# Kernel optimization log

Hardware: AMD Instinct MI355X
Metric: run time of the kernel (lower is better)

Reference implementation:

```python
import jax, jax.numpy as jnp
import numpy as np

EPS = 1.1920929e-07  # torch F.rms_norm default eps for fp32
D, NH, NKV, HD = 1024, 16, 4, 64
MLP_MULT, L = 3, 6           # L = num_layers // 2 shared blocks
VS, HS, LS, ROPE_B = 50257, 4096, 30.0, 10000.0
B, S = 2, 2048


def rmsn(x):
    return x * jax.lax.rsqrt(jnp.mean(jnp.square(x), -1, keepdims=True) + EPS)


def rope_tables(s):
    f = 1.0 / ROPE_B ** (jnp.arange(0, HD, 2, dtype=jnp.float32) / HD)
    fr = jnp.outer(jnp.arange(s, dtype=jnp.float32), f)  # [s, HD/2]
    return jnp.cos(fr), jnp.sin(fr)


def rot(x, c, s):
    h = x.shape[-1] // 2
    x1, x2 = x[..., :h], x[..., h:]
    return jnp.concatenate([x1 * c + x2 * s, -x1 * s + x2 * c], -1)


def attn(x, Wq, Wk, Wv, Wo, qg, cos, sin):
    b, s, d = x.shape
    q = (x @ Wq.T).reshape(b, s, NH, HD).swapaxes(1, 2)    # [b,nh,s,hd]
    k = (x @ Wk.T).reshape(b, s, NKV, HD).swapaxes(1, 2)   # [b,nkv,s,hd]
    v = (x @ Wv.T).reshape(b, s, NKV, HD).swapaxes(1, 2)
    q, k = rmsn(q), rmsn(k)                                # QK RMSNorm (no weight)
    c, si = cos[None, None], sin[None, None]
    q, k = rot(q, c, si), rot(k, c, si)
    q = q * qg[None, :, None, None]                        # per-head gate
    g = NH // NKV
    qr = q.reshape(b, NKV, g, s, HD)
    scores = jnp.einsum('bkgqd,bksd->bkgqs', qr, k) / jnp.sqrt(jnp.float32(HD))
    mask = jnp.tril(jnp.ones((s, s), bool))
    scores = jnp.where(mask, scores, -jnp.inf)
    p = jax.nn.softmax(scores, -1)
    y = jnp.einsum('bkgqs,bksd->bkgqd', p, v).reshape(b, NH, s, HD)
    y = y.swapaxes(1, 2).reshape(b, s, d)
    return y @ Wo.T


def mlp(x, Wf, Wo2):
    return jnp.square(jax.nn.relu(x @ Wf.T)) @ Wo2.T       # ReLU^2 MLP


def block(x, x0, p, cos, sin):
    Wq, Wk, Wv, Wo, qg, a_sc, m_sc, rm, Wf, Wo2 = p
    x = rm[0] * x + rm[1] * x0                             # learned residual mix
    x = x + a_sc * attn(rmsn(x), Wq, Wk, Wv, Wo, qg, cos, sin)
    x = x + m_sc * mlp(rmsn(x), Wf, Wo2)
    return x


def setup_inputs() -> dict:
    key = jax.random.key(0)
    ks = jax.random.split(key, 16)
    sd = 0.02
    return {
        'ids': jax.random.randint(ks[0], (B, S), 0, VS, dtype=jnp.int32),
        'y': jax.random.randint(ks[1], (B, S), 0, VS, dtype=jnp.int32),
        'u_emb': jax.random.normal(ks[2], (VS, D // 2), jnp.float32) * 0.02,
        'b_emb': jax.random.normal(ks[3], (HS, D // 2), jnp.float32) * 0.01,
        'Wq': jax.random.normal(ks[4], (L, D, D), jnp.float32) * sd,
        'Wk': jax.random.normal(ks[5], (L, NKV * HD, D), jnp.float32) * sd,
        'Wv': jax.random.normal(ks[6], (L, NKV * HD, D), jnp.float32) * sd,
        'Wo': jax.random.normal(ks[7], (L, D, D), jnp.float32) * sd,
        'qg': jnp.ones((L, NH), jnp.float32),
        'a_scale': jnp.ones((L, D), jnp.float32),
        'm_scale': jnp.ones((L, D), jnp.float32),
        'rm': jnp.stack([jnp.full((L, D), 0.7, jnp.float32), jnp.full((L, D), 0.3, jnp.float32)], 1),
        'Wf': jax.random.normal(ks[8], (L, MLP_MULT * D, D), jnp.float32) * sd,
        'Wo2': jax.random.normal(ks[9], (L, D, MLP_MULT * D), jnp.float32) * sd,
        'sw': jnp.ones((L, D), jnp.float32),
    }


def reference(ids, y, u_emb, b_emb, Wq, Wk, Wv, Wo, qg, a_scale, m_scale, rm, Wf, Wo2, sw):
    b, s = ids.shape
    # BigramHash embedding: (prev_id*VS + id) % HS, computed mod-HS to stay in int32
    pi = jnp.pad(ids[:, :-1], ((0, 0), (1, 0)))
    bi = (((pi % HS) * (VS % HS)) % HS + ids % HS) % HS
    h = jnp.concatenate([u_emb[ids], b_emb[bi]], -1)       # [b,s,D]
    h = rmsn(h)
    cos, sin = rope_tables(s)
    h0, sk = h, []
    for i in range(L):                                     # encoder half
        p = (Wq[i], Wk[i], Wv[i], Wo[i], qg[i], a_scale[i], m_scale[i], rm[i], Wf[i], Wo2[i])
        h = block(h, h0, p, cos, sin)
        sk.append(h)
    for i in range(L):                                     # decoder half (reversed blocks, skips)
        h = h + sw[i] * sk[L - 1 - i]
        j = L - 1 - i
        p = (Wq[j], Wk[j], Wv[j], Wo[j], qg[j], a_scale[j], m_scale[j], rm[j], Wf[j], Wo2[j])
        h = block(h, h0, p, cos, sin)
    h = rmsn(h)
    # tied bigram-hash head: out_weight = [u_emb | zeros]  ->  only first D/2 dims matter
    lg = h.reshape(-1, D)[:, :D // 2] @ u_emb.T            # [b*s, VS]
    lg = LS * jnp.tanh(lg / LS)                            # logit softcap
    logp = jax.nn.log_softmax(lg.astype(jnp.float32), -1)
    yf = y.reshape(-1)
    loss = -jnp.mean(jnp.take_along_axis(logp, yf[:, None], 1)[:, 0])
    return loss
```

## Files before the change

### kernel.cpp

```cpp
#include <hip/hip_runtime.h>
#include <cstdint>
#include <cstddef>

constexpr int   Dm    = 1024;
constexpr int   NHn   = 16;
constexpr int   NKVn  = 4;
constexpr int   HDn   = 64;
constexpr int   Ln    = 6;
constexpr int   Sn    = 2048;
constexpr int   Bn    = 2;
constexpr int   ROWS  = Bn * Sn;
constexpr int   VSn   = 50257;
constexpr int   HSn   = 4096;
constexpr float EPSF  = 1.1920929e-07f;
constexpr int   VCHUNK = 4096;
constexpr int   VPAD   = 50304;
constexpr float LOG2E  = 1.44269504f;

#define DEV __device__ __forceinline__

typedef __attribute__((ext_vector_type(8))) short bf16x8;
typedef __attribute__((ext_vector_type(4))) float f32x4;
using ush = unsigned short;

DEV ush f2bf(float f) {
    unsigned int u = __float_as_uint(f);
    u = (u + 0x7fffu + ((u >> 16) & 1u)) >> 16;
    return (ush)u;
}

DEV float b2f(ush v) {
    return __uint_as_float(((unsigned int)v) << 16);
}

DEV f32x4 mfma16(bf16x8 a, bf16x8 b, f32x4 c) {
    return __builtin_amdgcn_mfma_f32_16x16x32_bf16(a, b, c, 0, 0, 0);
}

DEV void llds16(const ush* g, ush* l) {
    __builtin_amdgcn_global_load_lds(
        (const __attribute__((address_space(1))) void*)g,
        (__attribute__((address_space(3))) void*)l, 16, 0, 0);
}

DEV void bar() {
    asm volatile("" ::: "memory");
    __builtin_amdgcn_s_barrier();
    asm volatile("" ::: "memory");
}

DEV float block_sum256(float v, float* red) {
#pragma unroll
    for (int off = 32; off; off >>= 1) v += __shfl_xor(v, off);
    __syncthreads();
    if ((threadIdx.x & 63) == 0) red[threadIdx.x >> 6] = v;
    __syncthreads();
    return red[0] + red[1] + red[2] + red[3];
}

DEV float block_max256(float v, float* red) {
#pragma unroll
    for (int off = 32; off; off >>= 1) v = fmaxf(v, __shfl_xor(v, off));
    __syncthreads();
    if ((threadIdx.x & 63) == 0) red[threadIdx.x >> 6] = v;
    __syncthreads();
    return fmaxf(fmaxf(red[0], red[1]), fmaxf(red[2], red[3]));
}

__global__ void rope_kernel(float* __restrict__ cb, float* __restrict__ sb) {
    int idx = blockIdx.x * 256 + threadIdx.x;
    if (idx >= Sn * 32) return;
    int t = idx >> 5, f = idx & 31;
    float freq = powf(10000.f, -(float)f * (1.f / 32.f));
    float ang  = (float)t * freq;
    cb[idx] = cosf(ang);
    sb[idx] = sinf(ang);
}

__global__ void cvt_bf16_kernel(const float* __restrict__ s, ush* __restrict__ d, int n4) {
    int i = blockIdx.x * 256 + threadIdx.x;
    if (i >= n4) return;
    float4 v = *(const float4*)(s + (size_t)i * 4);
    ushort4 o;
    o.x = f2bf(v.x); o.y = f2bf(v.y); o.z = f2bf(v.z); o.w = f2bf(v.w);
    *(ushort4*)(d + (size_t)i * 4) = o;
}

__global__ void zpad_kernel(ush* __restrict__ p, int n) {
    int i = blockIdx.x * 256 + threadIdx.x;
    if (i < n) p[i] = 0;
}

__global__ __launch_bounds__(256)
void embed_kernel(const int* __restrict__ ids, const float* __restrict__ ue,
                  const float* __restrict__ be, float* __restrict__ h,
                  float* __restrict__ h0) {
    __shared__ float red[4];
    int r = blockIdx.x;
    int s = r % Sn;
    int id = ids[r];
    int prev = (s == 0) ? 0 : ids[r - 1];
    int bi = ((prev % HSn) * (VSn % HSn) % HSn + id % HSn) % HSn;
    int tid = threadIdx.x;
    float vals[4];
    float ss = 0.f;
#pragma unroll
    for (int t = 0; t < 4; ++t) {
        int j = tid + t * 256;
        float v = (j < 512) ? ue[(size_t)id * 512 + j]
                            : be[(size_t)bi * 512 + (j - 512)];
        vals[t] = v; ss += v * v;
    }
    ss = block_sum256(ss, red);
    float rinv = rsqrtf(ss * (1.f / Dm) + EPSF);
#pragma unroll
    for (int t = 0; t < 4; ++t) {
        int j = tid + t * 256;
        float v = vals[t] * rinv;
        h [(size_t)r * Dm + j] = v;
        h0[(size_t)r * Dm + j] = v;
    }
}

template<bool SKIP>
__global__ __launch_bounds__(256)
void resmix_kernel(float* __restrict__ h, const float* __restrict__ h0,
                   const float* __restrict__ rm0, ush* __restrict__ xnb,
                   const ush* __restrict__ skb, const float* __restrict__ sw) {
    __shared__ float red[4];
    int r = blockIdx.x, tid = threadIdx.x;
    const float* rm1 = rm0 + Dm;
    float vals[4]; float ss = 0.f;
#pragma unroll
    for (int t = 0; t < 4; ++t) {
        int j = tid + t * 256;
        size_t o = (size_t)r * Dm + j;
        float base = h[o];
        if (SKIP) base = fmaf(sw[j], b2f(skb[o]), base);
        float v = rm0[j] * base + rm1[j] * h0[o];
        vals[t] = v; ss += v * v;
        h[o] = v;
    }
    ss = block_sum256(ss, red);
    float rinv = rsqrtf(ss * (1.f / Dm) + EPSF);
#pragma unroll
    for (int t = 0; t < 4; ++t)
        xnb[(size_t)r * Dm + tid + t * 256] = f2bf(vals[t] * rinv);
}

__global__ __launch_bounds__(256)
void rmsn_kernel(const float* __restrict__ x, ush* __restrict__ out) {
    __shared__ float red[4];
    int r = blockIdx.x, tid = threadIdx.x;
    float vals[4]; float ss = 0.f;
#pragma unroll
    for (int t = 0; t < 4; ++t) {
        float v = x[(size_t)r * Dm + tid + t * 256];
        vals[t] = v; ss += v * v;
    }
    ss = block_sum256(ss, red);
    float rinv = rsqrtf(ss * (1.f / Dm) + EPSF);
#pragma unroll
    for (int t = 0; t < 4; ++t)
        out[(size_t)r * Dm + tid + t * 256] = f2bf(vals[t] * rinv);
}

template<int TM, int MODE>
__global__ __launch_bounds__(256)
void gemm_k(const ush* __restrict__ A, const ush* __restrict__ B,
            ush* __restrict__ C, int M, int N, int K,
            int lda, int ldb, int ldc,
            float* __restrict__ hres, const float* __restrict__ sc,
            ush* __restrict__ dup) {
    constexpr int ASZ = TM * 32;
    __shared__ __align__(16) ush As[3][ASZ];
    __shared__ __align__(16) ush Bs[3][128 * 32];
    const int m0 = blockIdx.x * TM, n0 = blockIdx.y * 128;
    const int tid  = threadIdx.x;
    const int w    = tid >> 6, lane = tid & 63;
    const int l15  = lane & 15, quad = lane >> 4;
    const int wr   = w >> 1, wc = w & 1;
    constexpr int NI = TM / 32;

    const int srow = lane >> 2;
    const int schs = (lane & 3) ^ ((srow >> 1) & 3);
    const ush* Ag;
    int aoff;
    if constexpr (TM == 128) {
        Ag   = A + (size_t)(m0 + w * 32 + srow) * lda + schs * 8;
        aoff = w * 1024;
    } else {
        Ag   = A + (size_t)(m0 + w * 16 + srow) * lda + schs * 8;
        aoff = w * 512;
    }
    const ush* Bg  = B + (size_t)(n0 + w * 32 + srow) * ldb + schs * 8;
    const int boff = w * 1024;

    auto stage = [&](int buf, int k0) {
        llds16(Ag + k0, &As[buf][aoff]);
        if constexpr (TM == 128) llds16(Ag + k0 + 16 * lda, &As[buf][aoff + 512]);
        llds16(Bg + k0,            &Bs[buf][boff]);
        llds16(Bg + k0 + 16 * ldb, &Bs[buf][boff + 512]);
    };

    f32x4 acc[NI][4] = {};
    const int nt = K >> 5;

    stage(0, 0);
    if (nt > 1) {
        stage(1, 32);
        if constexpr (TM == 128) asm volatile("s_waitcnt vmcnt(4)" ::: "memory");
        else                     asm volatile("s_waitcnt vmcnt(3)" ::: "memory");
    } else {
        asm volatile("s_waitcnt vmcnt(0)" ::: "memory");
    }
    bar();

    const int cso = (quad ^ ((l15 >> 1) & 3)) * 8;
    int bcur = 0;
    for (int t = 0; t < nt; ++t) {
        if (t + 2 < nt) {
            int bn = bcur >= 1 ? bcur - 1 : 2;
            stage(bn, (t + 2) * 32);
        }
        bf16x8 af[NI], bfv[4];
#pragma unroll
        for (int i = 0; i < NI; ++i)
            af[i] = *(const bf16x8*)&As[bcur][(wr * (TM / 2) + i * 16 + l15) * 32 + cso];
#pragma unroll
        for (int j = 0; j < 4; ++j)
            bfv[j] = *(const bf16x8*)&Bs[bcur][(wc * 64 + j * 16 + l15) * 32 + cso];
#pragma unroll
        for (int i = 0; i < NI; ++i)
#pragma unroll
            for (int j = 0; j < 4; ++j)
                acc[i][j] = mfma16(af[i], bfv[j], acc[i][j]);
        if (t + 2 < nt) {
            if constexpr (TM == 128) asm volatile("s_waitcnt vmcnt(4)" ::: "memory");
            else                     asm volatile("s_waitcnt vmcnt(3)" ::: "memory");
        } else {
            asm volatile("s_waitcnt vmcnt(0)" ::: "memory");
        }
        bar();
        bcur = bcur == 2 ? 0 : bcur + 1;
    }

#pragma unroll
    for (int i = 0; i < NI; ++i) {
#pragma unroll
        for (int j = 0; j < 4; ++j) {
            int row = m0 + wr * (TM / 2) + i * 16 + quad * 4;
            int col = n0 + wc * 64 + j * 16 + l15;
#pragma unroll
            for (int r = 0; r < 4; ++r) {
                float v = acc[i][j][r];
                if (MODE == 1) { v = fmaxf(v, 0.f); v = v * v; }
                else if (MODE == 2) {
                    float ax = fabsf(v) * (1.f / 30.f);
                    float e  = __expf(-2.f * ax);
                    float t  = (1.f - e) / (1.f + e);
                    v = copysignf(t * 30.f, v);
                }
                if (MODE == 3) {
                    size_t o = (size_t)(row + r) * ldc + col;
                    float nv = fmaf(sc[col], v, hres[o]);
                    hres[o] = nv;
                    if (dup) dup[o] = f2bf(nv);
                } else {
                    C[(size_t)(row + r) * ldc + col] = f2bf(v);
                }
            }
        }
    }
}

__global__ __launch_bounds__(256)
void qknorm_rope_kernel(const ush* __restrict__ in,
                        ush* __restrict__ qout, ush* __restrict__ kout,
                        const float* __restrict__ cosb, const float* __restrict__ sinb,
                        const float* __restrict__ qg) {
    int idx  = blockIdx.x * 4 + (threadIdx.x >> 6);
    int lane = threadIdx.x & 63;
    int t, hh, in_off;
    ush* outp; int out_ld;
    bool isq = idx < ROWS * NHn;
    if (isq) { t = idx >> 4; hh = idx & 15; in_off = hh * 64; outp = qout; out_ld = 1024; }
    else { int i2 = idx - ROWS * NHn; t = i2 >> 2; hh = i2 & 3; in_off = 1024 + hh * 64; outp = kout; out_ld = 256; }
    int sidx = t % Sn;
    float x = b2f(in[(size_t)t * 1536 + in_off + lane]);
    float ss = x * x;
#pragma unroll
    for (int off = 32; off; off >>= 1) ss += __shfl_xor(ss, off);
    float xn = x * rsqrtf(ss * (1.f / HDn) + EPSF);
    float partner = __shfl_xor(xn, 32);
    int f = lane & 31;
    float c  = cosb[sidx * 32 + f];
    float sv = sinb[sidx * 32 + f];
    float o = (lane < 32) ? fmaf(xn, c, partner * sv)
                          : fmaf(xn, c, -partner * sv);
    if (isq) o *= qg[hh] * (0.125f * LOG2E);
    outp[(size_t)t * out_ld + hh * 64 + lane] = f2bf(o);
}

__global__ __launch_bounds__(256)
void vtrans_kernel(const ush* __restrict__ in, ush* __restrict__ out) {
    __shared__ ush tile[32][33];
    int s0 = blockIdx.x * 32;
    int c0 = blockIdx.y * 32;
    int i = threadIdx.x >> 5;
    int j = threadIdx.x & 31;
#pragma unroll
    for (int k = 0; k < 4; ++k)
        tile[i + k * 8][j] = in[(size_t)(s0 + i + k * 8) * 1536 + 1280 + c0 + j];
    __syncthreads();
#pragma unroll
    for (int k = 0; k < 4; ++k)
        out[(size_t)(c0 + i + k * 8) * (size_t)ROWS + s0 + j] = tile[j][i + k * 8];
}

__global__ __launch_bounds__(256)
void attn_mfma_kernel(const ush* __restrict__ qb,
                      const ush* __restrict__ kb,
                      const ush* __restrict__ vt,
                      ush* __restrict__ opart,
                      float* __restrict__ lpart,
                      const float* __restrict__ qgl) {
    __shared__ __align__(16) ush Ks[64 * 72];
    __shared__ __align__(16) ush Vs[64 * 72];
    __shared__ __align__(16) unsigned int PsD[128 * 36];
    const int pair = blockIdx.x % 40;
    const int bh   = blockIdx.x / 40;
    const int h    = bh & 15;
    const int b    = bh >> 4;
    const int g    = (pair >= 24) ? 3 : (pair >= 12) ? 2 : (pair >= 4) ? 1 : 0;
    const int off_p = pair - 2 * g * (g + 1);
    const int t    = 4 * g + off_p / (g + 1);
    const int c    = off_p % (g + 1);
    const int kvh  = h >> 2;
    const int w    = threadIdx.x >> 6, lane = threadIdx.x & 63;
    const int l15  = lane & 15, quad = lane >> 4;
    const int q0   = t * 128;
    const int k_lo = c * 512;
    const int k_hi_full = (t + 1) * 128;
    const int k_hi = (k_lo + 512 < k_hi_full) ? (k_lo + 512) : k_hi_full;
    const int nblk = (k_hi - k_lo) >> 6;
    const float mfix = 8.f * fabsf(qgl[h]) * LOG2E;

    bf16x8 qf[2][2];
    {
        size_t qr = (size_t)(b * Sn + q0 + w * 32 + l15) * 1024 + h * 64;
        qf[0][0] = *(const bf16x8*)(qb + qr + quad * 8);
        qf[0][1] = *(const bf16x8*)(qb + qr + 32 + quad * 8);
        qf[1][0] = *(const bf16x8*)(qb + qr + 16 * 1024 + quad * 8);
        qf[1][1] = *(const bf16x8*)(qb + qr + 16 * 1024 + 32 + quad * 8);
    }
    f32x4 Oacc[2][4] = {};
    float lsum[2][4] = {{0.f,0.f,0.f,0.f},{0.f,0.f,0.f,0.f}};

    const int rrS = threadIdx.x >> 3, chS = threadIdx.x & 7;
    const size_t kbase = (size_t)(b * Sn) * 256 + kvh * 64;
    const size_t vbase = (size_t)(kvh * 64) * (size_t)ROWS + b * Sn;

    uint4 kr0 = *(const uint4*)(kb + kbase + (size_t)(k_lo + rrS) * 256 + chS * 8);
    uint4 kr1 = *(const uint4*)(kb + kbase + (size_t)(k_lo + rrS + 32) * 256 + chS * 8);
    uint4 vr0 = *(const uint4*)(vt + vbase + (size_t)rrS * ROWS + k_lo + chS * 8);
    uint4 vr1 = *(const uint4*)(vt + vbase + (size_t)(rrS + 32) * ROWS + k_lo + chS * 8);

    for (int kb_i = 0; kb_i < nblk; ++kb_i) {
        const int k0 = k_lo + kb_i * 64;
        __syncthreads();
        *(uint4*)&Ks[rrS * 72 + chS * 8]        = kr0;
        *(uint4*)&Ks[(rrS + 32) * 72 + chS * 8] = kr1;
        *(uint4*)&Vs[rrS * 72 + chS * 8]        = vr0;
        *(uint4*)&Vs[(rrS + 32) * 72 + chS * 8] = vr1;
        __syncthreads();
        if (kb_i + 1 < nblk) {
            int k0n = k0 + 64;
            kr0 = *(const uint4*)(kb + kbase + (size_t)(k0n + rrS) * 256 + chS * 8);
            kr1 = *(const uint4*)(kb + kbase + (size_t)(k0n + rrS + 32) * 256 + chS * 8);
            vr0 = *(const uint4*)(vt + vbase + (size_t)rrS * ROWS + k0n + chS * 8);
            vr1 = *(const uint4*)(vt + vbase + (size_t)(rrS + 32) * ROWS + k0n + chS * 8);
        }

        f32x4 S0[4] = {}, S1[4] = {};
#pragma unroll
        for (int cc = 0; cc < 4; ++cc) {
            bf16x8 kf0 = *(const bf16x8*)&Ks[(cc * 16 + l15) * 72 + quad * 8];
            bf16x8 kf1 = *(const bf16x8*)&Ks[(cc * 16 + l15) * 72 + 32 + quad * 8];
            S0[cc] = mfma16(qf[0][0], kf0, S0[cc]);
            S0[cc] = mfma16(qf[0][1], kf1, S0[cc]);
            S1[cc] = mfma16(qf[1][0], kf0, S1[cc]);
            S1[cc] = mfma16(qf[1][1], kf1, S1[cc]);
        }

#pragma unroll
        for (int f = 0; f < 2; ++f) {
            f32x4* S = f ? S1 : S0;
            const int qbF = q0 + w * 32 + f * 16;
            if (k0 + 63 > qbF) {
#pragma unroll
                for (int cc = 0; cc < 4; ++cc) {
                    int key = k0 + cc * 16 + l15;
#pragma unroll
                    for (int r = 0; r < 4; ++r)
                        if (key > qbF + quad * 4 + r) S[cc][r] = -INFINITY;
                }
            }
#pragma unroll
            for (int cc = 0; cc < 4; ++cc)
#pragma unroll
                for (int r = 0; r < 4; ++r) {
                    float p = exp2f(S[cc][r] - mfix);
                    S[cc][r] = p;
                    lsum[f][r] += p;
                }
            const int prow = w * 32 + f * 16 + quad * 4;
#pragma unroll
            for (int cp = 0; cp < 2; ++cp)
#pragma unroll
                for (int r = 0; r < 4; ++r) {
                    unsigned int pk = __builtin_amdgcn_perm(
                        __float_as_uint(S[cp + 2][r]), __float_as_uint(S[cp][r]),
                        0x07060302u);
                    PsD[(prow + r) * 36 + cp * 16 + l15] = pk;
                }
        }

#pragma unroll
        for (int f = 0; f < 2; ++f) {
            const int prow = w * 32 + f * 16 + l15;
            unsigned int d[8];
            *(uint4*)&d[0] = *(const uint4*)&PsD[prow * 36 + quad * 8];
            *(uint4*)&d[4] = *(const uint4*)&PsD[prow * 36 + quad * 8 + 4];
            unsigned int lo[4], hi[4];
#pragma unroll
            for (int tt = 0; tt < 4; ++tt) {
                lo[tt] = __builtin_amdgcn_perm(d[2 * tt + 1], d[2 * tt], 0x05040100u);
                hi[tt] = __builtin_amdgcn_perm(d[2 * tt + 1], d[2 * tt], 0x07060302u);
            }
            bf16x8 pf0 = *(const bf16x8*)lo;
            bf16x8 pf1 = *(const bf16x8*)hi;
#pragma unroll
            for (int dt = 0; dt < 4; ++dt) {
                bf16x8 vf0 = *(const bf16x8*)&Vs[(dt * 16 + l15) * 72 + quad * 8];
                bf16x8 vf1 = *(const bf16x8*)&Vs[(dt * 16 + l15) * 72 + 32 + quad * 8];
                Oacc[f][dt] = mfma16(pf0, vf0, Oacc[f][dt]);
                Oacc[f][dt] = mfma16(pf1, vf1, Oacc[f][dt]);
            }
        }
    }

#pragma unroll
    for (int f = 0; f < 2; ++f) {
#pragma unroll
        for (int m = 1; m <= 8; m <<= 1)
#pragma unroll
            for (int r = 0; r < 4; ++r)
                lsum[f][r] += __shfl_xor(lsum[f][r], m);
#pragma unroll
        for (int r = 0; r < 4; ++r) {
            int token = b * Sn + q0 + w * 32 + f * 16 + quad * 4 + r;
            if (l15 == 0)
                lpart[((size_t)c * ROWS + token) * NHn + h] = lsum[f][r];
#pragma unroll
            for (int dt = 0; dt < 4; ++dt)
                opart[((size_t)c * ROWS + token) * 1024 + h * 64 + dt * 16 + l15]
                    = f2bf(Oacc[f][dt][r]);
        }
    }
}

__global__ __launch_bounds__(256)
void attn_combine_kernel(const ush* __restrict__ opart,
                         const float* __restrict__ lpart,
                         ush* __restrict__ attb) {
    int token = blockIdx.x;
    int j = threadIdx.x * 4;
    int head = j >> 6;
    int nc = ((token % Sn) >> 9) + 1;
    float a0 = 0.f, a1 = 0.f, a2 = 0.f, a3 = 0.f, l = 0.f;
    for (int cc = 0; cc < nc; ++cc) {
        ushort4 o4 = *(const ushort4*)(opart + ((size_t)cc * ROWS + token) * 1024 + j);
        a0 += b2f(o4.x); a1 += b2f(o4.y); a2 += b2f(o4.z); a3 += b2f(o4.w);
        l  += lpart[((size_t)cc * ROWS + token) * NHn + head];
    }
    float rin = 1.f / l;
    ushort4 out;
    out.x = f2bf(a0 * rin); out.y = f2bf(a1 * rin);
    out.z = f2bf(a2 * rin); out.w = f2bf(a3 * rin);
    *(ushort4*)(attb + (size_t)token * 1024 + j) = out;
}

__global__ void loss_init_kernel(float* __restrict__ m, float* __restrict__ s,
                                 float* __restrict__ tg) {
    int i = blockIdx.x * 256 + threadIdx.x;
    if (i < ROWS) { m[i] = -INFINITY; s[i] = 0.f; tg[i] = 0.f; }
}

__global__ __launch_bounds__(256)
void chunk_reduce_kernel(const ush* __restrict__ Cc, int Nc, int c0,
                         const int* __restrict__ y, float* __restrict__ m,
                         float* __restrict__ s, float* __restrict__ tg) {
    __shared__ float red[4];
    int r = blockIdx.x, tid = threadIdx.x;
    const ush* row = Cc + (size_t)r * VCHUNK;
    float v[16];
    float mx = -INFINITY;
#pragma unroll
    for (int t = 0; t < 16; ++t) {
        int j = tid + t * 256;
        v[t] = (j < Nc) ? b2f(row[j]) : -INFINITY;
        mx = fmaxf(mx, v[t]);
    }
    mx = block_max256(mx, red);
    float se = 0.f;
#pragma unroll
    for (int t = 0; t < 16; ++t)
        se += __expf(v[t] - mx);
    se = block_sum256(se, red);
    if (tid == 0) {
        float mo = m[r];
        float mn = fmaxf(mo, mx);
        s[r] = s[r] * __expf(mo - mn) + se * __expf(mx - mn);
        m[r] = mn;
        int t = y[r] - c0;
        if (t >= 0 && t < Nc) tg[r] = b2f(row[t]);
    }
}

__global__ __launch_bounds__(256)
void loss_final_kernel(const float* __restrict__ m, const float* __restrict__ s,
                       const float* __restrict__ tg, float* __restrict__ out) {
    __shared__ float red[4];
    float part = 0.f;
    for (int r = threadIdx.x; r < ROWS; r += 256)
        part += m[r] + logf(s[r]) - tg[r];
    part = block_sum256(part, red);
    if (threadIdx.x == 0) out[0] = part * (1.f / ROWS);
}

extern "C" void kernel_launch(void* const* d_in, const int* in_sizes, int n_in,
                              void* d_out, int out_size, void* d_ws, size_t ws_size,
                              hipStream_t stream) {
    const int*   ids = (const int*)d_in[0];
    const int*   yv  = (const int*)d_in[1];
    const float* ue  = (const float*)d_in[2];
    const float* be  = (const float*)d_in[3];
    const float* Wq  = (const float*)d_in[4];
    const float* Wk  = (const float*)d_in[5];
    const float* Wv  = (const float*)d_in[6];
    const float* Wo  = (const float*)d_in[7];
    const float* qg  = (const float*)d_in[8];
    const float* asc = (const float*)d_in[9];
    const float* msc = (const float*)d_in[10];
    const float* rm  = (const float*)d_in[11];
    const float* Wf  = (const float*)d_in[12];
    const float* Wo2 = (const float*)d_in[13];
    const float* sw  = (const float*)d_in[14];
    (void)in_sizes; (void)n_in; (void)out_size; (void)ws_size;

    char* wsb = (char*)d_ws;
    size_t off = 0;
    auto alloc = [&](size_t bytes) {
        void* p = (void*)(wsb + off);
        off += ((bytes + 255) & ~size_t(255));
        return p;
    };
    float* h    = (float*)alloc((size_t)ROWS * Dm * 4);
    float* h0   = (float*)alloc((size_t)ROWS * Dm * 4);
    float* cosb = (float*)alloc((size_t)Sn * 32 * 4);
    float* sinb = (float*)alloc((size_t)Sn * 32 * 4);
    float* mrow = (float*)alloc(ROWS * 4);
    float* srow = (float*)alloc(ROWS * 4);
    float* tgv  = (float*)alloc(ROWS * 4);
    float* lpart= (float*)alloc((size_t)4 * ROWS * NHn * 4);
    ush* skb  = (ush*)alloc((size_t)Ln * ROWS * Dm * 2);
    ush* xnb  = (ush*)alloc((size_t)ROWS * Dm * 2);
    ush* qkvb = (ush*)alloc((size_t)ROWS * 1536 * 2);
    ush* hidb = (ush*)alloc((size_t)ROWS * 3 * Dm * 2);
    ush* opart = qkvb;
    ush* qbf  = (ush*)alloc((size_t)ROWS * Dm * 2);
    ush* kbf  = (ush*)alloc((size_t)ROWS * 256 * 2);
    ush* vtb  = (ush*)alloc((size_t)256 * ROWS * 2);
    ush* attb = (ush*)alloc((size_t)ROWS * Dm * 2);
    ush* wall = (ush*)alloc((size_t)Ln * 8704 * 1024 * 2);
    ush* ueb  = (ush*)alloc((size_t)VPAD * 512 * 2);
    ush* chunk = skb;

    auto cvt = [&](const float* s, ush* d, size_t n) {
        int n4 = (int)(n / 4);
        cvt_bf16_kernel<<<(n4 + 255) / 256, 256, 0, stream>>>(s, d, n4);
    };

    for (int l = 0; l < Ln; ++l) {
        ush* wl = wall + (size_t)l * 8704 * 1024;
        cvt(Wq + (size_t)l * Dm * Dm,      wl,              (size_t)Dm * Dm);
        cvt(Wk + (size_t)l * 256 * Dm,     wl + 1024 * Dm,  (size_t)256 * Dm);
        cvt(Wv + (size_t)l * 256 * Dm,     wl + 1280 * Dm,  (size_t)256 * Dm);
        cvt(Wo + (size_t)l * Dm * Dm,      wl + 1536 * Dm,  (size_t)Dm * Dm);
        cvt(Wf + (size_t)l * 3 * Dm * Dm,  wl + 2560 * Dm,  (size_t)3 * Dm * Dm);
        cvt(Wo2 + (size_t)l * 3 * Dm * Dm, wl + 5632 * Dm,  (size_t)3 * Dm * Dm);
    }
    cvt(ue, ueb, (size_t)VSn * 512);
    zpad_kernel<<<((VPAD - VSn) * 512 + 255) / 256, 256, 0, stream>>>(
        ueb + (size_t)VSn * 512, (VPAD - VSn) * 512);

    rope_kernel<<<(Sn * 32 + 255) / 256, 256, 0, stream>>>(cosb, sinb);
    embed_kernel<<<ROWS, 256, 0, stream>>>(ids, ue, be, h, h0);

    auto run_block = [&](int l, ush* dup, const ush* skip, const float* swv) {
        ush* wl    = wall + (size_t)l * 8704 * 1024;
        ush* wqkvb = wl;
        ush* wob   = wl + (size_t)1536 * 1024;
        ush* wfb   = wl + (size_t)2560 * 1024;
        ush* wo2b  = wl + (size_t)5632 * 1024;

        if (skip)
            resmix_kernel<true><<<ROWS, 256, 0, stream>>>(
                h, h0, rm + (size_t)l * 2 * Dm, xnb, skip, swv);
        else
            resmix_kernel<false><<<ROWS, 256, 0, stream>>>(
                h, h0, rm + (size_t)l * 2 * Dm, xnb, nullptr, nullptr);
        gemm_k<64, 0><<<dim3(ROWS / 64, 1536 / 128), 256, 0, stream>>>(
            xnb, wqkvb, qkvb, ROWS, 1536, Dm, Dm, Dm, 1536, nullptr, nullptr, nullptr);
        qknorm_rope_kernel<<<ROWS * (NHn + NKVn) / 4, 256, 0, stream>>>(
            qkvb, qbf, kbf, cosb, sinb, qg + (size_t)l * NHn);
        vtrans_kernel<<<dim3(ROWS / 32, 8), 256, 0, stream>>>(qkvb, vtb);
        attn_mfma_kernel<<<Bn * NHn * 40, 256, 0, stream>>>(
            qbf, kbf, vtb, opart, lpart, qg + (size_t)l * NHn);
        attn_combine_kernel<<<ROWS, 256, 0, stream>>>(opart, lpart, attb);
        gemm_k<64, 3><<<dim3(ROWS / 64, Dm / 128), 256, 0, stream>>>(
            attb, wob, nullptr, ROWS, Dm, Dm, Dm, Dm, Dm,
            h, asc + (size_t)l * Dm, nullptr);
        rmsn_kernel<<<ROWS, 256, 0, stream>>>(h, xnb);
        gemm_k<128, 1><<<dim3(ROWS / 128, 3 * Dm / 128), 256, 0, stream>>>(
            xnb, wfb, hidb, ROWS, 3 * Dm, Dm, Dm, Dm, 3 * Dm, nullptr, nullptr, nullptr);
        gemm_k<64, 3><<<dim3(ROWS / 64, Dm / 128), 256, 0, stream>>>(
            hidb, wo2b, nullptr, ROWS, Dm, 3 * Dm, 3 * Dm, 3 * Dm, Dm,
            h, msc + (size_t)l * Dm, dup);
    };

    for (int l = 0; l < Ln; ++l)
        run_block(l, skb + (size_t)l * ROWS * Dm, nullptr, nullptr);
    for (int i = 0; i < Ln; ++i) {
        int j = Ln - 1 - i;
        run_block(j, nullptr, skb + (size_t)j * ROWS * Dm, sw + (size_t)i * Dm);
    }

    rmsn_kernel<<<ROWS, 256, 0, stream>>>(h, xnb);
    loss_init_kernel<<<(ROWS + 255) / 256, 256, 0, stream>>>(mrow, srow, tgv);
    for (int c0 = 0; c0 < VSn; c0 += VCHUNK) {
        int Nc = (VSn - c0 < VCHUNK) ? (VSn - c0) : VCHUNK;
        int Ng = (VPAD - c0 < VCHUNK) ? (VPAD - c0) : VCHUNK;
        gemm_k<128, 2><<<dim3(ROWS / 128, Ng / 128), 256, 0, stream>>>(
            xnb, ueb + (size_t)c0 * 512, chunk, ROWS, Ng, 512, Dm, 512, VCHUNK,
            nullptr, nullptr, nullptr);
        chunk_reduce_kernel<<<ROWS, 256, 0, stream>>>(chunk, Nc, c0, yv, mrow, srow, tgv);
    }
    loss_final_kernel<<<1, 256, 0, stream>>>(mrow, srow, tgv, (float*)d_out);
}
```

Before: 4.078 ms.

## Deepen GEMM prefetch pipeline, unroll buffer rotation, and swizzle workgroup order

Reworks the bf16 MFMA GEMM main loop to use more shared-memory stages (four buffers with three tiles in flight for TM=64, three buffers for TM=128). The buffer-rotation loop is fully unrolled with compile-time buffer indices and vmcnt waits sized to the new depth, and an explicit lgkmcnt wait plus sched_barrier is added before each barrier. Workgroup IDs are remapped in groups of eight to change the tile traversal order, aimed at better cache locality. The goal is to hide more global-load latency and cut per-iteration index overhead, at the cost of extra LDS per block, which may reduce occupancy.

```diff
diff --git a/kernel.cpp b/kernel.cpp
--- a/kernel.cpp
+++ b/kernel.cpp
@@ -172,10 +172,20 @@
             int lda, int ldb, int ldc,
             float* __restrict__ hres, const float* __restrict__ sc,
             ush* __restrict__ dup) {
-    constexpr int ASZ = TM * 32;
-    __shared__ __align__(16) ush As[3][ASZ];
-    __shared__ __align__(16) ush Bs[3][128 * 32];
-    const int m0 = blockIdx.x * TM, n0 = blockIdx.y * 128;
+    constexpr int DEPTH = (TM == 64) ? 3 : 2;
+    constexpr int NBUF  = DEPTH + 1;
+    constexpr int LPS   = (TM == 128) ? 4 : 3;
+    constexpr int ASZ   = TM * 32;
+    __shared__ __align__(16) ush As[NBUF][ASZ];
+    __shared__ __align__(16) ush Bs[NBUF][128 * 32];
+
+    const int gx  = gridDim.x;
+    const int nwg = gx * gridDim.y;
+    const int bl  = blockIdx.y * gx + blockIdx.x;
+    const int chunk = nwg >> 3;
+    const int swb = (bl & 7) * chunk + (bl >> 3);
+    const int m0 = (swb % gx) * TM, n0 = (swb / gx) * 128;
+
     const int tid  = threadIdx.x;
     const int w    = tid >> 6, lane = tid & 63;
     const int l15  = lane & 15, quad = lane >> 4;
@@ -203,46 +213,77 @@
         llds16(Bg + k0 + 16 * ldb, &Bs[buf][boff + 512]);
     };
 
+    auto waitN = [&](int stages) {
+        if (stages >= 2) {
+            if constexpr (LPS == 3) asm volatile("s_waitcnt vmcnt(6)" ::: "memory");
+            else                    asm volatile("s_waitcnt vmcnt(8)" ::: "memory");
+        } else if (stages == 1) {
+            if constexpr (LPS == 3) asm volatile("s_waitcnt vmcnt(3)" ::: "memory");
+            else                    asm volatile("s_waitcnt vmcnt(4)" ::: "memory");
+        } else {
+            asm volatile("s_waitcnt vmcnt(0)" ::: "memory");
+        }
+    };
+
+    auto dsdone = [&]() {
+        asm volatile("s_waitcnt lgkmcnt(0)" ::: "memory");
+        __builtin_amdgcn_sched_barrier(0);
+    };
+
     f32x4 acc[NI][4] = {};
     const int nt = K >> 5;
-
-    stage(0, 0);
-    if (nt > 1) {
-        stage(1, 32);
-        if constexpr (TM == 128) asm volatile("s_waitcnt vmcnt(4)" ::: "memory");
-        else                     asm volatile("s_waitcnt vmcnt(3)" ::: "memory");
-    } else {
-        asm volatile("s_waitcnt vmcnt(0)" ::: "memory");
-    }
-    bar();
-
     const int cso = (quad ^ ((l15 >> 1) & 3)) * 8;
-    int bcur = 0;
-    for (int t = 0; t < nt; ++t) {
-        if (t + 2 < nt) {
-            int bn = bcur >= 1 ? bcur - 1 : 2;
-            stage(bn, (t + 2) * 32);
-        }
+
+    auto computeStep = [&](int u) {
         bf16x8 af[NI], bfv[4];
 #pragma unroll
         for (int i = 0; i < NI; ++i)
-            af[i] = *(const bf16x8*)&As[bcur][(wr * (TM / 2) + i * 16 + l15) * 32 + cso];
+            af[i] = *(const bf16x8*)&As[u][(wr * (TM / 2) + i * 16 + l15) * 32 + cso];
 #pragma unroll
         for (int j = 0; j < 4; ++j)
-            bfv[j] = *(const bf16x8*)&Bs[bcur][(wc * 64 + j * 16 + l15) * 32 + cso];
+            bfv[j] = *(const bf16x8*)&Bs[u][(wc * 64 + j * 16 + l15) * 32 + cso];
 #pragma unroll
         for (int i = 0; i < NI; ++i)
 #pragma unroll
             for (int j = 0; j < 4; ++j)
                 acc[i][j] = mfma16(af[i], bfv[j], acc[i][j]);
-        if (t + 2 < nt) {
-            if constexpr (TM == 128) asm volatile("s_waitcnt vmcnt(4)" ::: "memory");
-            else                     asm volatile("s_waitcnt vmcnt(3)" ::: "memory");
-        } else {
-            asm volatile("s_waitcnt vmcnt(0)" ::: "memory");
-        }
-        bar();
-        bcur = bcur == 2 ? 0 : bcur + 1;
+    };
+
+    stage(0, 0);
+    if (nt > 1) stage(1, 32);
+    if constexpr (DEPTH == 3) { if (nt > 2) stage(2, 64); }
+    {
+        int pre = nt < DEPTH ? nt : DEPTH;
+        waitN(pre - 1);
+    }
+    bar();
+
+    int t0 = 0;
+    for (; t0 + NBUF + DEPTH <= nt; t0 += NBUF) {
+#pragma unroll
+        for (int u = 0; u < NBUF; ++u) {
+            const int t = t0 + u;
+            stage((u + DEPTH) % NBUF, (t + DEPTH) * 32);
+            computeStep(u);
+            waitN(DEPTH - 1);
+            dsdone();
+            bar();
+        }
+    }
+    for (; t0 < nt; t0 += NBUF) {
+#pragma unroll
+        for (int u = 0; u < NBUF; ++u) {
+            const int t = t0 + u;
+            if (t < nt) {
+                if (t + DEPTH < nt) stage((u + DEPTH) % NBUF, (t + DEPTH) * 32);
+                computeStep(u);
+                int rem = nt - 1 - t;
+                int keep = (t + DEPTH < nt) ? (DEPTH - 1) : (rem > 0 ? rem - 1 : 0);
+                waitN(keep);
+                dsdone();
+                bar();
+            }
+        }
     }
 
 #pragma unroll
```

After: 4.679 ms. 14.7% more time.
